# Optimization experiments

Measured on AMD Instinct MI355X. Metric: run time of the kernel, lower is better.

Reference implementation:

```python
import jax, jax.numpy as jnp
import numpy as np

LN_EPS = 1e-5


def setup_inputs() -> dict:
    key = jax.random.key(0)
    ks = jax.random.split(key, 4)
    B, d, rank, z = 4096, 1024, 16, 1024
    hd = jax.random.normal(ks[0], (B, d), dtype=jnp.float32)
    hp = jax.random.normal(ks[1], (B, d), dtype=jnp.float32)
    U = jax.random.normal(ks[2], (rank, d, z), dtype=jnp.float32) * 0.02
    V = jax.random.normal(ks[3], (rank, d, z), dtype=jnp.float32) * 0.02
    gamma = jnp.ones((z,), dtype=jnp.float32)
    beta = jnp.zeros((z,), dtype=jnp.float32)
    return {"hd": hd, "hp": hp, "U": U, "V": V, "gamma": gamma, "beta": beta}


def reference(hd, hp, U, V, gamma, beta):
    # Low-rank Tucker bilinear fusion: sum_r (hd @ U[r]) * (hp @ V[r])
    u = jnp.einsum('bd,rdz->brz', hd, U)   # [B, rank, z]
    v = jnp.einsum('bd,rdz->brz', hp, V)   # [B, rank, z]
    z = jax.nn.relu(jnp.einsum('brz,brz->bz', u, v))  # fused mul+sum over rank
    # Dropout in eval mode = identity. LayerNorm over last dim.
    mean = jnp.mean(z, axis=-1, keepdims=True)
    var = jnp.var(z, axis=-1, keepdims=True)
    zn = (z - mean) * jax.lax.rsqrt(var + LN_EPS)
    return zn * gamma + beta
```

## Files before the change

kernel.cpp:

```cpp
#include <hip/hip_runtime.h>


typedef unsigned short u16;
typedef __attribute__((ext_vector_type(8)))  short bf16x8;
typedef __attribute__((ext_vector_type(16))) float f32x16;

constexpr int Bq = 4096;
constexpr int D  = 1024;
constexpr int Zq = 1024;
constexpr int Rk = 16;

typedef const __attribute__((address_space(1))) void* gas_t;
typedef __attribute__((address_space(3))) void* las_t;

__device__ __forceinline__ u16 f2b(float f) {
  union { float f; unsigned u; } c; c.f = f;
  unsigned r = (c.u + 0x7FFFu + ((c.u >> 16) & 1u)) >> 16;
  return (u16)r;
}
__device__ __forceinline__ float b2f(u16 h) {
  union { unsigned u; float f; } c; c.u = ((unsigned)h) << 16; return c.f;
}

__global__ __launch_bounds__(256) void fm_pack_A(const float* __restrict__ src,
                                                 u16* __restrict__ dst) {
  const int g  = blockIdx.x * 256 + threadIdx.x;
  const int c  = g & 1023;
  const int kt = (g >> 10) & 15;
  const int bx = g >> 14;
  const int l   = c & 63;
  const int ks  = (c >> 6) & 3;
  const int mfb = c >> 8;
  const int row = bx * 128 + mfb * 32 + (l & 31);
  const int kb  = kt * 64 + ks * 16 + ((l >> 5) << 3);
  const float* s = src + (size_t)row * D + kb;
  const float4 f0 = *(const float4*)s;
  const float4 f1 = *(const float4*)(s + 4);
  union { u16 h[8]; uint4 u; } o;
  o.h[0] = f2b(f0.x); o.h[1] = f2b(f0.y); o.h[2] = f2b(f0.z); o.h[3] = f2b(f0.w);
  o.h[4] = f2b(f1.x); o.h[5] = f2b(f1.y); o.h[6] = f2b(f1.z); o.h[7] = f2b(f1.w);
  *(uint4*)(dst + (size_t)g * 8) = o.u;
}

__global__ __launch_bounds__(256) void fm_pack_B(const float* __restrict__ src,
                                                 u16* __restrict__ dst) {
  const int g  = blockIdx.x * 256 + threadIdx.x;
  const int c  = g & 1023;
  const int kt = (g >> 10) & 15;
  const int jt = (g >> 14) & 7;
  const int r  = g >> 17;
  const int l   = c & 63;
  const int ks  = (c >> 6) & 3;
  const int nfb = c >> 8;
  const int col = jt * 128 + nfb * 32 + (l & 31);
  const int kg  = kt * 64 + ks * 16 + ((l >> 5) << 3);
  const float* s = src + (size_t)r * (D * Zq) + (size_t)kg * Zq + col;
  union { u16 h[8]; uint4 u; } o;
  #pragma unroll
  for (int e = 0; e < 8; ++e) o.h[e] = f2b(s[(size_t)e * Zq]);
  *(uint4*)(dst + (size_t)g * 8) = o.u;
}

#define GLDS(src, dst) __builtin_amdgcn_global_load_lds((gas_t)(src), (las_t)(dst), 16, 0, 0)
#define MFMA32(a, b, c) __builtin_amdgcn_mfma_f32_32x32x16_bf16(a, b, c, 0, 0, 0)

#define STAGE_A(buf, st) do {                                                    \
    const int _kt = (st) & 15;                                                   \
    GLDS(hdp + _kt * 8192 + c0 * 8, &sT[buf][0][c0 * 8]);                        \
    GLDS(hdp + _kt * 8192 + c1 * 8, &sT[buf][0][c1 * 8]);                        \
    GLDS(hpp + _kt * 8192 + c0 * 8, &sT[buf][1][c0 * 8]);                        \
    GLDS(hpp + _kt * 8192 + c1 * 8, &sT[buf][1][c1 * 8]);                        \
  } while (0)

#define STAGE_B(buf, st) do {                                                    \
    const int _kt = (st) & 15;                                                   \
    const u16* _u = Ub + (size_t)((st) >> 4) * rstride + _kt * 8192;             \
    const u16* _v = Vb + (size_t)((st) >> 4) * rstride + _kt * 8192;             \
    GLDS(_u + c0 * 8, &sT[buf][2][c0 * 8]);                                      \
    GLDS(_u + c1 * 8, &sT[buf][2][c1 * 8]);                                      \
    GLDS(_v + c0 * 8, &sT[buf][3][c0 * 8]);                                      \
    GLDS(_v + c1 * 8, &sT[buf][3][c1 * 8]);                                      \
  } while (0)

#define COMPUTE(buf) do {                                                        \
    const u16* tA = sT[buf][role];                                               \
    const u16* tB = sT[buf][2 + role];                                           \
    _Pragma("unroll")                                                            \
    for (int ks = 0; ks < 4; ++ks) {                                             \
      bf16x8 a0 = *(const bf16x8*)(tA + (((wm * 2 + 0) * 4 + ks) * 64 + lane) * 8); \
      bf16x8 a1 = *(const bf16x8*)(tA + (((wm * 2 + 1) * 4 + ks) * 64 + lane) * 8); \
      bf16x8 b0 = *(const bf16x8*)(tB + (((wn * 2 + 0) * 4 + ks) * 64 + lane) * 8); \
      bf16x8 b1 = *(const bf16x8*)(tB + (((wn * 2 + 1) * 4 + ks) * 64 + lane) * 8); \
      __builtin_amdgcn_s_setprio(1);                                             \
      aw[0][0] = MFMA32(a0, b0, aw[0][0]);                                       \
      aw[0][1] = MFMA32(a0, b1, aw[0][1]);                                       \
      aw[1][0] = MFMA32(a1, b0, aw[1][0]);                                       \
      aw[1][1] = MFMA32(a1, b1, aw[1][1]);                                       \
      __builtin_amdgcn_s_setprio(0);                                             \
    }                                                                            \
  } while (0)

__global__ __launch_bounds__(512, 2) void fused_bilinear(
    const u16* __restrict__ hdf, const u16* __restrict__ hpf,
    const u16* __restrict__ Uf, const u16* __restrict__ Vf,
    float* __restrict__ out)
{
  __shared__ __align__(16) u16 sT[2][4][8192];

  const int tid  = threadIdx.x;
  const int lane = tid & 63;
  const int wid  = tid >> 6;
  const int role = wid >> 2;
  const int w4   = wid & 3;
  const int wm   = w4 >> 1;
  const int wn   = w4 & 1;

  const int bx = blockIdx.x;
  const int jt = blockIdx.y;

  const u16* hdp = hdf + (size_t)bx * 16 * 8192;
  const u16* hpp = hpf + (size_t)bx * 16 * 8192;
  const u16* Ub  = Uf + (size_t)jt * 16 * 8192;
  const u16* Vb  = Vf + (size_t)jt * 16 * 8192;
  const size_t rstride = (size_t)8 * 16 * 8192;

  const int c0 = tid;
  const int c1 = tid + 512;

  f32x16 acc[2][2], aw[2][2];
  #pragma unroll
  for (int mf = 0; mf < 2; ++mf)
    #pragma unroll
    for (int nf = 0; nf < 2; ++nf) {
      #pragma unroll
      for (int i = 0; i < 16; ++i) { acc[mf][nf][i] = 0.f; aw[mf][nf][i] = 0.f; }
    }

  unsigned* exch = (unsigned*)&sT[0][2][0];

  STAGE_A(0, 0);
  STAGE_B(0, 0);
  __syncthreads();

  #pragma unroll 1
  for (int it = 0; it < 128; ++it) {
    const int s0 = it * 2;
    const int s1 = s0 + 1;

    STAGE_A(1, s1);
    STAGE_B(1, s1);
    COMPUTE(0);
    __syncthreads();

    const bool bound = ((s1 & 15) == 15);
    if (s1 < 255) {
      STAGE_A(0, s1 + 1);
      if (!bound) STAGE_B(0, s1 + 1);
    }
    COMPUTE(1);
    if (bound) {
      __syncthreads();
      if (role) {
        #pragma unroll
        for (int mf = 0; mf < 2; ++mf)
          #pragma unroll
          for (int nf = 0; nf < 2; ++nf) {
            const int f = mf * 2 + nf;
            #pragma unroll
            for (int rp = 0; rp < 8; ++rp) {
              const unsigned lo = f2b(aw[mf][nf][2 * rp]);
              const unsigned hi = f2b(aw[mf][nf][2 * rp + 1]);
              exch[((w4 * 4 + f) * 8 + rp) * 64 + lane] = lo | (hi << 16);
            }
          }
      }
      __syncthreads();
      if (!role) {
        #pragma unroll
        for (int mf = 0; mf < 2; ++mf)
          #pragma unroll
          for (int nf = 0; nf < 2; ++nf) {
            const int f = mf * 2 + nf;
            #pragma unroll
            for (int rp = 0; rp < 8; ++rp) {
              const unsigned w = exch[((w4 * 4 + f) * 8 + rp) * 64 + lane];
              acc[mf][nf][2 * rp]     += aw[mf][nf][2 * rp]     * b2f((u16)(w & 0xFFFFu));
              acc[mf][nf][2 * rp + 1] += aw[mf][nf][2 * rp + 1] * b2f((u16)(w >> 16));
            }
          }
      }
      #pragma unroll
      for (int mf = 0; mf < 2; ++mf)
        #pragma unroll
        for (int nf = 0; nf < 2; ++nf)
          #pragma unroll
          for (int i = 0; i < 16; ++i) aw[mf][nf][i] = 0.f;
      __syncthreads();
      if (s1 < 255) STAGE_B(0, s1 + 1);
      __syncthreads();
    } else {
      __syncthreads();
    }
  }

  if (!role) {
    const int brow = bx * 128 + wm * 64;
    const int jcol = jt * 128 + wn * 64;
    #pragma unroll
    for (int mf = 0; mf < 2; ++mf)
      #pragma unroll
      for (int nf = 0; nf < 2; ++nf) {
        #pragma unroll
        for (int i = 0; i < 16; ++i) {
          const int row = brow + mf * 32 + (i & 3) + 8 * (i >> 2) + 4 * (lane >> 5);
          const int col = jcol + nf * 32 + (lane & 31);
          out[(size_t)row * Zq + col] = acc[mf][nf][i];
        }
      }
  }
}

__global__ __launch_bounds__(256) void ln_rows(float* __restrict__ out,
    const float* __restrict__ gamma, const float* __restrict__ beta)
{
  const int row = blockIdx.x;
  const int t = threadIdx.x;
  float* o = out + (size_t)row * Zq;
  float4 v = ((const float4*)o)[t];
  v.x = fmaxf(v.x, 0.f); v.y = fmaxf(v.y, 0.f);
  v.z = fmaxf(v.z, 0.f); v.w = fmaxf(v.w, 0.f);
  float s = v.x + v.y + v.z + v.w;
  float q = v.x * v.x + v.y * v.y + v.z * v.z + v.w * v.w;
  #pragma unroll
  for (int off = 32; off > 0; off >>= 1) {
    s += __shfl_xor(s, off);
    q += __shfl_xor(q, off);
  }
  __shared__ float ss[4], sq[4];
  if ((t & 63) == 0) { ss[t >> 6] = s; sq[t >> 6] = q; }
  __syncthreads();
  s = ss[0] + ss[1] + ss[2] + ss[3];
  q = sq[0] + sq[1] + sq[2] + sq[3];
  const float mean = s * (1.f / Zq);
  float var = q * (1.f / Zq) - mean * mean;
  var = fmaxf(var, 0.f);
  const float rstd = rsqrtf(var + 1e-5f);
  const float4 g  = ((const float4*)gamma)[t];
  const float4 bb = ((const float4*)beta)[t];
  v.x = (v.x - mean) * rstd * g.x + bb.x;
  v.y = (v.y - mean) * rstd * g.y + bb.y;
  v.z = (v.z - mean) * rstd * g.z + bb.z;
  v.w = (v.w - mean) * rstd * g.w + bb.w;
  ((float4*)o)[t] = v;
}

__global__ __launch_bounds__(256) void fallback_bilinear(
    const float* __restrict__ hd, const float* __restrict__ hp,
    const float* __restrict__ U, const float* __restrict__ V,
    float* __restrict__ out)
{
  const int j  = blockIdx.x * 256 + threadIdx.x;
  const int b0 = blockIdx.y * 8;
  float acc[8] = {0.f, 0.f, 0.f, 0.f, 0.f, 0.f, 0.f, 0.f};
  for (int r = 0; r < Rk; ++r) {
    float u[8] = {0.f}, v[8] = {0.f};
    const float* Up = U + (size_t)r * (D * Zq) + j;
    const float* Vp = V + (size_t)r * (D * Zq) + j;
    for (int k = 0; k < D; ++k) {
      const float uu = Up[(size_t)k * Zq];
      const float vv = Vp[(size_t)k * Zq];
      #pragma unroll
      for (int bi = 0; bi < 8; ++bi) {
        u[bi] = fmaf(hd[(size_t)(b0 + bi) * D + k], uu, u[bi]);
        v[bi] = fmaf(hp[(size_t)(b0 + bi) * D + k], vv, v[bi]);
      }
    }
    #pragma unroll
    for (int bi = 0; bi < 8; ++bi) acc[bi] += u[bi] * v[bi];
  }
  #pragma unroll
  for (int bi = 0; bi < 8; ++bi)
    out[(size_t)(b0 + bi) * Zq + j] = acc[bi];
}

extern "C" void kernel_launch(void* const* d_in, const int* in_sizes, int n_in,
                              void* d_out, int out_size, void* d_ws, size_t ws_size,
                              hipStream_t stream) {
  const float* hd    = (const float*)d_in[0];
  const float* hp    = (const float*)d_in[1];
  const float* U     = (const float*)d_in[2];
  const float* V     = (const float*)d_in[3];
  const float* gamma = (const float*)d_in[4];
  const float* beta  = (const float*)d_in[5];
  float* out = (float*)d_out;

  const size_t need = 80ull << 20;
  if (ws_size >= need) {
    u16* hdf = (u16*)d_ws;
    u16* hpf = hdf + (size_t)Bq * D;
    u16* Ufm = hpf + (size_t)Bq * D;
    u16* Vfm = Ufm + (size_t)Rk * D * Zq;

    fm_pack_A<<<2048, 256, 0, stream>>>(hd, hdf);
    fm_pack_A<<<2048, 256, 0, stream>>>(hp, hpf);
    fm_pack_B<<<8192, 256, 0, stream>>>(U, Ufm);
    fm_pack_B<<<8192, 256, 0, stream>>>(V, Vfm);
    fused_bilinear<<<dim3(32, 8), 512, 0, stream>>>(hdf, hpf, Ufm, Vfm, out);
  } else {
    fallback_bilinear<<<dim3(Zq / 256, Bq / 8), 256, 0, stream>>>(hd, hp, U, V, out);
  }
  ln_rows<<<Bq, 256, 0, stream>>>(out, gamma, beta);
}
```

Before: 351.8 us.

## Prefetch two stages ahead with explicit vmcnt waits and dedicated exchange buffer

Restructures the double-buffered main loop so each stage's loads are issued two steps ahead. Partial waits (s_waitcnt vmcnt(8)) plus raw s_barrier and sched_barrier fences replace __syncthreads, so the next stage's global-to-LDS copies stay in flight during compute. The rank-boundary exchange moves to a separate LDS buffer, split into two halves, so it no longer aliases the B tile and no longer forces B staging to be deferred. This costs extra LDS, which may reduce occupancy at two blocks per CU, and relies on manual waitcnt counts being correct.

New measurement: 375.9 us. 6.8% more time.

```diff
diff --git a/kernel.cpp b/kernel.cpp
--- a/kernel.cpp
+++ b/kernel.cpp
@@ -63,6 +63,8 @@
 
 #define GLDS(src, dst) __builtin_amdgcn_global_load_lds((gas_t)(src), (las_t)(dst), 16, 0, 0)
 #define MFMA32(a, b, c) __builtin_amdgcn_mfma_f32_32x32x16_bf16(a, b, c, 0, 0, 0)
+#define SFENCE() __builtin_amdgcn_sched_barrier(0)
+#define BAR()    __builtin_amdgcn_s_barrier()
 
 #define STAGE_A(buf, st) do {                                                    \
     const int _kt = (st) & 15;                                                   \
@@ -106,6 +108,7 @@
     float* __restrict__ out)
 {
   __shared__ __align__(16) u16 sT[2][4][8192];
+  __shared__ __align__(16) unsigned exch2[4096];
 
   const int tid  = threadIdx.x;
   const int lane = tid & 63;
@@ -136,70 +139,76 @@
       for (int i = 0; i < 16; ++i) { acc[mf][nf][i] = 0.f; aw[mf][nf][i] = 0.f; }
     }
 
-  unsigned* exch = (unsigned*)&sT[0][2][0];
-
-  STAGE_A(0, 0);
-  STAGE_B(0, 0);
-  __syncthreads();
+  STAGE_A(0, 0); STAGE_B(0, 0);
+  STAGE_A(1, 1); STAGE_B(1, 1);
+  SFENCE();
+  asm volatile("s_waitcnt vmcnt(8)" ::: "memory");
+  SFENCE();
+  BAR(); SFENCE();
 
   #pragma unroll 1
   for (int it = 0; it < 128; ++it) {
-    const int s0 = it * 2;
-    const int s1 = s0 + 1;
-
-    STAGE_A(1, s1);
-    STAGE_B(1, s1);
+    const int s0 = it * 2, s1 = s0 + 1;
+
     COMPUTE(0);
-    __syncthreads();
-
+    SFENCE(); BAR(); SFENCE();
+    if (s0 + 2 < 256) {
+      STAGE_A(0, s0 + 2); STAGE_B(0, s0 + 2);
+      SFENCE();
+      asm volatile("s_waitcnt vmcnt(8)" ::: "memory");
+    } else {
+      SFENCE();
+      asm volatile("s_waitcnt vmcnt(0)" ::: "memory");
+    }
+    SFENCE(); BAR(); SFENCE();
+
+    COMPUTE(1);
+    SFENCE(); BAR(); SFENCE();
     const bool bound = ((s1 & 15) == 15);
-    if (s1 < 255) {
-      STAGE_A(0, s1 + 1);
-      if (!bound) STAGE_B(0, s1 + 1);
-    }
-    COMPUTE(1);
     if (bound) {
-      __syncthreads();
-      if (role) {
-        #pragma unroll
-        for (int mf = 0; mf < 2; ++mf)
+      #pragma unroll
+      for (int g = 0; g < 2; ++g) {
+        if (role) {
           #pragma unroll
-          for (int nf = 0; nf < 2; ++nf) {
-            const int f = mf * 2 + nf;
+          for (int nf = 0; nf < 2; ++nf)
             #pragma unroll
             for (int rp = 0; rp < 8; ++rp) {
-              const unsigned lo = f2b(aw[mf][nf][2 * rp]);
-              const unsigned hi = f2b(aw[mf][nf][2 * rp + 1]);
-              exch[((w4 * 4 + f) * 8 + rp) * 64 + lane] = lo | (hi << 16);
+              const unsigned lo = f2b(aw[g][nf][2 * rp]);
+              const unsigned hi = f2b(aw[g][nf][2 * rp + 1]);
+              exch2[((w4 * 2 + nf) * 8 + rp) * 64 + lane] = lo | (hi << 16);
             }
-          }
-      }
-      __syncthreads();
-      if (!role) {
-        #pragma unroll
-        for (int mf = 0; mf < 2; ++mf)
+          asm volatile("s_waitcnt lgkmcnt(0)" ::: "memory");
+        }
+        SFENCE(); BAR(); SFENCE();
+        if (!role) {
           #pragma unroll
-          for (int nf = 0; nf < 2; ++nf) {
-            const int f = mf * 2 + nf;
+          for (int nf = 0; nf < 2; ++nf)
             #pragma unroll
             for (int rp = 0; rp < 8; ++rp) {
-              const unsigned w = exch[((w4 * 4 + f) * 8 + rp) * 64 + lane];
-              acc[mf][nf][2 * rp]     += aw[mf][nf][2 * rp]     * b2f((u16)(w & 0xFFFFu));
-              acc[mf][nf][2 * rp + 1] += aw[mf][nf][2 * rp + 1] * b2f((u16)(w >> 16));
+              const unsigned w = exch2[((w4 * 2 + nf) * 8 + rp) * 64 + lane];
+              acc[g][nf][2 * rp]     += aw[g][nf][2 * rp]     * b2f((u16)(w & 0xFFFFu));
+              acc[g][nf][2 * rp + 1] += aw[g][nf][2 * rp + 1] * b2f((u16)(w >> 16));
             }
-          }
+        }
+        if (g == 0) { SFENCE(); BAR(); SFENCE(); }
       }
+    }
+    if (s1 + 2 < 256) {
+      STAGE_A(1, s1 + 2); STAGE_B(1, s1 + 2);
+      SFENCE();
+      asm volatile("s_waitcnt vmcnt(8)" ::: "memory");
+    } else {
+      SFENCE();
+      asm volatile("s_waitcnt vmcnt(0)" ::: "memory");
+    }
+    SFENCE(); BAR(); SFENCE();
+    if (bound) {
       #pragma unroll
       for (int mf = 0; mf < 2; ++mf)
         #pragma unroll
         for (int nf = 0; nf < 2; ++nf)
           #pragma unroll
           for (int i = 0; i < 16; ++i) aw[mf][nf][i] = 0.f;
-      __syncthreads();
-      if (s1 < 255) STAGE_B(0, s1 + 1);
-      __syncthreads();
-    } else {
-      __syncthreads();
     }
   }
 
```

## Use dedicated LDS exchange buffer and merge pack launches

Applied to the files above, without the earlier changes.

Adds a separate shared-memory buffer for the cross-role bf16 exchange of per-rank partial products, so the B tile prefetch no longer has to be deferred at rank boundaries. The exchange is split into two halves with raw s_barrier plus explicit lgkmcnt waits, replacing several full __syncthreads. The four pack kernels are also merged into two launches using blockIdx.y to pick the tensor. Extra LDS (16KB) may reduce occupancy at 2 blocks per CU.

Result: slower. 359.4 us (+2.2%).

```diff
diff --git a/kernel.cpp b/kernel.cpp
--- a/kernel.cpp
+++ b/kernel.cpp
@@ -22,8 +22,12 @@
   union { unsigned u; float f; } c; c.u = ((unsigned)h) << 16; return c.f;
 }
 
-__global__ __launch_bounds__(256) void fm_pack_A(const float* __restrict__ src,
-                                                 u16* __restrict__ dst) {
+__global__ __launch_bounds__(256) void fm_pack_A2(const float* __restrict__ sA,
+                                                  const float* __restrict__ sB,
+                                                  u16* __restrict__ dA,
+                                                  u16* __restrict__ dB) {
+  const float* src = blockIdx.y ? sB : sA;
+  u16* dst = blockIdx.y ? dB : dA;
   const int g  = blockIdx.x * 256 + threadIdx.x;
   const int c  = g & 1023;
   const int kt = (g >> 10) & 15;
@@ -42,8 +46,12 @@
   *(uint4*)(dst + (size_t)g * 8) = o.u;
 }
 
-__global__ __launch_bounds__(256) void fm_pack_B(const float* __restrict__ src,
-                                                 u16* __restrict__ dst) {
+__global__ __launch_bounds__(256) void fm_pack_B2(const float* __restrict__ sU,
+                                                  const float* __restrict__ sV,
+                                                  u16* __restrict__ dU,
+                                                  u16* __restrict__ dV) {
+  const float* src = blockIdx.y ? sV : sU;
+  u16* dst = blockIdx.y ? dV : dU;
   const int g  = blockIdx.x * 256 + threadIdx.x;
   const int c  = g & 1023;
   const int kt = (g >> 10) & 15;
@@ -63,6 +71,7 @@
 
 #define GLDS(src, dst) __builtin_amdgcn_global_load_lds((gas_t)(src), (las_t)(dst), 16, 0, 0)
 #define MFMA32(a, b, c) __builtin_amdgcn_mfma_f32_32x32x16_bf16(a, b, c, 0, 0, 0)
+#define BAR() __builtin_amdgcn_s_barrier()
 
 #define STAGE_A(buf, st) do {                                                    \
     const int _kt = (st) & 15;                                                   \
@@ -106,6 +115,7 @@
     float* __restrict__ out)
 {
   __shared__ __align__(16) u16 sT[2][4][8192];
+  __shared__ __align__(16) unsigned exch2[4096];
 
   const int tid  = threadIdx.x;
   const int lane = tid & 63;
@@ -136,8 +146,6 @@
       for (int i = 0; i < 16; ++i) { acc[mf][nf][i] = 0.f; aw[mf][nf][i] = 0.f; }
     }
 
-  unsigned* exch = (unsigned*)&sT[0][2][0];
-
   STAGE_A(0, 0);
   STAGE_B(0, 0);
   __syncthreads();
@@ -152,42 +160,39 @@
     COMPUTE(0);
     __syncthreads();
 
-    const bool bound = ((s1 & 15) == 15);
     if (s1 < 255) {
       STAGE_A(0, s1 + 1);
-      if (!bound) STAGE_B(0, s1 + 1);
+      STAGE_B(0, s1 + 1);
     }
     COMPUTE(1);
+    const bool bound = ((s1 & 15) == 15);
     if (bound) {
-      __syncthreads();
-      if (role) {
-        #pragma unroll
-        for (int mf = 0; mf < 2; ++mf)
+      #pragma unroll
+      for (int g = 0; g < 2; ++g) {
+        if (role) {
           #pragma unroll
-          for (int nf = 0; nf < 2; ++nf) {
-            const int f = mf * 2 + nf;
+          for (int nf = 0; nf < 2; ++nf)
             #pragma unroll
             for (int rp = 0; rp < 8; ++rp) {
-              const unsigned lo = f2b(aw[mf][nf][2 * rp]);
-              const unsigned hi = f2b(aw[mf][nf][2 * rp + 1]);
-              exch[((w4 * 4 + f) * 8 + rp) * 64 + lane] = lo | (hi << 16);
+              const unsigned lo = f2b(aw[g][nf][2 * rp]);
+              const unsigned hi = f2b(aw[g][nf][2 * rp + 1]);
+              exch2[((w4 * 2 + nf) * 8 + rp) * 64 + lane] = lo | (hi << 16);
             }
-          }
-      }
-      __syncthreads();
-      if (!role) {
-        #pragma unroll
-        for (int mf = 0; mf < 2; ++mf)
+          asm volatile("s_waitcnt lgkmcnt(0)" ::: "memory");
+        }
+        BAR();
+        if (!role) {
           #pragma unroll
-          for (int nf = 0; nf < 2; ++nf) {
-            const int f = mf * 2 + nf;
+          for (int nf = 0; nf < 2; ++nf)
             #pragma unroll
             for (int rp = 0; rp < 8; ++rp) {
-              const unsigned w = exch[((w4 * 4 + f) * 8 + rp) * 64 + lane];
-              acc[mf][nf][2 * rp]     += aw[mf][nf][2 * rp]     * b2f((u16)(w & 0xFFFFu));
-              acc[mf][nf][2 * rp + 1] += aw[mf][nf][2 * rp + 1] * b2f((u16)(w >> 16));
+              const unsigned w = exch2[((w4 * 2 + nf) * 8 + rp) * 64 + lane];
+              acc[g][nf][2 * rp]     += aw[g][nf][2 * rp]     * b2f((u16)(w & 0xFFFFu));
+              acc[g][nf][2 * rp + 1] += aw[g][nf][2 * rp + 1] * b2f((u16)(w >> 16));
             }
-          }
+          asm volatile("s_waitcnt lgkmcnt(0)" ::: "memory");
+        }
+        if (g == 0) BAR();
       }
       #pragma unroll
       for (int mf = 0; mf < 2; ++mf)
@@ -195,12 +200,8 @@
         for (int nf = 0; nf < 2; ++nf)
           #pragma unroll
           for (int i = 0; i < 16; ++i) aw[mf][nf][i] = 0.f;
-      __syncthreads();
-      if (s1 < 255) STAGE_B(0, s1 + 1);
-      __syncthreads();
-    } else {
-      __syncthreads();
     }
+    __syncthreads();
   }
 
   if (!role) {
@@ -301,10 +302,8 @@
     u16* Ufm = hpf + (size_t)Bq * D;
     u16* Vfm = Ufm + (size_t)Rk * D * Zq;
 
-    fm_pack_A<<<2048, 256, 0, stream>>>(hd, hdf);
-    fm_pack_A<<<2048, 256, 0, stream>>>(hp, hpf);
-    fm_pack_B<<<8192, 256, 0, stream>>>(U, Ufm);
-    fm_pack_B<<<8192, 256, 0, stream>>>(V, Vfm);
+    fm_pack_A2<<<dim3(2048, 2), 256, 0, stream>>>(hd, hp, hdf, hpf);
+    fm_pack_B2<<<dim3(8192, 2), 256, 0, stream>>>(U, V, Ufm, Vfm);
     fused_bilinear<<<dim3(32, 8), 512, 0, stream>>>(hdf, hpf, Ufm, Vfm, out);
   } else {
     fallback_bilinear<<<dim3(Zq / 256, Bq / 8), 256, 0, stream>>>(hd, hp, U, V, out);
```
